# Kernel optimization log

Measured on AMD Instinct MI355X. Metric: run time of the kernel, lower is better.

Reference implementation:

```python
import jax, jax.numpy as jnp
import numpy as np

N_SAMPLES = 32768
N_ATOMS = 1024
ATOM_LEN = 2048
N_TO_KEEP = 1024


def fft_convolve(a, b):
    """Linear convolution via FFT: zero-pad both to 2n, multiply spectra, truncate to n."""
    n = a.shape[-1]
    a = jnp.pad(a, [(0, 0)] * (a.ndim - 1) + [(0, n)])
    b = jnp.pad(b, [(0, 0)] * (b.ndim - 1) + [(0, n)])
    spec = jnp.fft.rfft(a, axis=-1) * jnp.fft.rfft(b, axis=-1)  # broadcast (B,1024,2n//2+1)
    return jnp.fft.irfft(spec, axis=-1)[..., :n]


def sparsify(x, n_to_keep):
    """Keep the top-k raw values over the flattened per-batch feature map; zero the rest."""
    shp = x.shape
    flat = x.reshape(shp[0], -1)                       # (B, 1024*32768)
    vals, idx = jax.lax.top_k(flat, n_to_keep)         # (B, k)
    out = jnp.zeros_like(flat).at[jnp.arange(shp[0])[:, None], idx].set(vals)
    return out.reshape(shp)


def setup_inputs() -> dict:
    key = jax.random.key(0)
    k1, k2 = jax.random.split(key)
    x = jax.random.normal(k1, (2, 1, N_SAMPLES), dtype=jnp.float32)
    # atoms initialized uniform(-0.01, 0.01) in the original module
    atoms = jax.random.uniform(k2, (1, N_ATOMS, ATOM_LEN), dtype=jnp.float32,
                               minval=-0.01, maxval=0.01)
    return {"x": x, "atoms": atoms}


def reference(x, atoms):
    padded = jnp.pad(atoms, ((0, 0), (0, 0), (0, N_SAMPLES - atoms.shape[-1])))  # (1,1024,32768)
    fm = fft_convolve(x, padded)            # (B, 1024, 32768)
    fm = sparsify(fm, N_TO_KEEP)
    recon = fft_convolve(fm, padded)        # (B, 1024, 32768)
    recon = jnp.sum(recon, axis=1, keepdims=True)  # (B, 1, 32768)
    return recon
```

## Files before the change

kernel.cpp:

```cpp
#include <hip/hip_runtime.h>
#include <hip/hip_bf16.h>

#define NS    32768
#define NA    1024
#define AL    2048
#define KKEEP 1024
#define CAPC  (512*1024)

struct Cand { float v; unsigned idx; };

typedef short  short8  __attribute__((ext_vector_type(8)));
typedef short  short4v __attribute__((ext_vector_type(4)));
typedef float  f32x4   __attribute__((ext_vector_type(4)));


__device__ inline unsigned short f2bf(float f) {
    union { float f; unsigned u; } v; v.f = f;
    unsigned r = v.u + 0x7fffu + ((v.u >> 16) & 1u);
    return (unsigned short)(r >> 16);
}

__global__ void prep_kernel(const float* __restrict__ x, const float* __restrict__ atoms,
                            float* __restrict__ psum, float* __restrict__ hdr,
                            unsigned* __restrict__ candCnt, unsigned* __restrict__ done,
                            unsigned short* __restrict__ ab16) {
    __shared__ float red[12];
    __shared__ int   isLast;
    const int bid = blockIdx.x;
    const int tid = threadIdx.x;
    const int i   = bid * 256 + tid;
    float4 f = *(const float4*)(atoms + (size_t)i * 4);
    ushort4 o;
    o.x = f2bf(f.x); o.y = f2bf(f.y); o.z = f2bf(f.z); o.w = f2bf(f.w);
    *(ushort4*)(ab16 + (size_t)i * 4) = o;
    float sa  = f.x*f.x + f.y*f.y + f.z*f.z + f.w*f.w;
    float sx0 = 0.f, sx1 = 0.f;
    if (i < 16384) {
        float4 xv = *(const float4*)(x + (size_t)i * 4);
        float s = xv.x*xv.x + xv.y*xv.y + xv.z*xv.z + xv.w*xv.w;
        if (i < 8192) sx0 = s; else sx1 = s;
    }
    #pragma unroll
    for (int off = 32; off >= 1; off >>= 1) {
        sa  += __shfl_down(sa , off);
        sx0 += __shfl_down(sx0, off);
        sx1 += __shfl_down(sx1, off);
    }
    if ((tid & 63) == 0) {
        red[(tid >> 6) * 3 + 0] = sa;
        red[(tid >> 6) * 3 + 1] = sx0;
        red[(tid >> 6) * 3 + 2] = sx1;
    }
    __syncthreads();
    if (tid == 0) {
        psum[bid * 3 + 0] = red[0] + red[3] + red[6] + red[9];
        psum[bid * 3 + 1] = red[1] + red[4] + red[7] + red[10];
        psum[bid * 3 + 2] = red[2] + red[5] + red[8] + red[11];
        __threadfence();
        unsigned old = atomicAdd(done, 1u);
        isLast = (((old + 1u) & 2047u) == 0u) ? 1 : 0;
    }
    __syncthreads();
    if (!isLast) return;

    __threadfence();
    float pa = 0.f, p0s = 0.f, p1s = 0.f;
    for (int j = tid; j < 2048; j += 256) {
        pa  += psum[3 * j + 0];
        p0s += psum[3 * j + 1];
        p1s += psum[3 * j + 2];
    }
    #pragma unroll
    for (int off = 32; off >= 1; off >>= 1) {
        pa  += __shfl_down(pa , off);
        p0s += __shfl_down(p0s, off);
        p1s += __shfl_down(p1s, off);
    }
    __syncthreads();
    if ((tid & 63) == 0) {
        red[(tid >> 6) * 3 + 0] = pa;
        red[(tid >> 6) * 3 + 1] = p0s;
        red[(tid >> 6) * 3 + 2] = p1s;
    }
    __syncthreads();
    if (tid == 0) {
        hdr[0] = red[1] + red[4] + red[7] + red[10];
        hdr[1] = red[2] + red[5] + red[8] + red[11];
        hdr[2] = red[0] + red[3] + red[6] + red[9];
        candCnt[0] = 0u; candCnt[1] = 0u;
    }
}

#define XRW      2175
#define XRSTRIDE 2192
#define XRB      4384
#define NCPY     4
#define SA_BUF   16384

__device__ inline void gload_lds16(const unsigned short* g, unsigned char* lds) {
    __builtin_amdgcn_global_load_lds((const __attribute__((address_space(1))) void*)g,
                                     (__attribute__((address_space(3))) void*)lds,
                                     16, 0, 0);
}

__global__ __launch_bounds__(256, 3)
void fm_kernel(const float* __restrict__ x,
               const unsigned short* __restrict__ ab16,
               const float* __restrict__ hdr, unsigned* __restrict__ candCnt,
               Cand* __restrict__ cand, unsigned cap)
{
    __shared__ __align__(16) unsigned char  sA[2 * SA_BUF];
    __shared__ __align__(16) unsigned short sXR[NCPY * XRSTRIDE];

    const int bid = blockIdx.x;
    const int b   = bid >> 11;
    const int rem = bid & 2047;
    const int a0  = (rem >> 8) * 128;
    const int t0  = (rem & 255) * 128;

    const int tid  = threadIdx.x;
    const int lane = tid & 63;
    const int wid  = tid >> 6;
    const int wm   = wid >> 1;
    const int wn   = wid & 1;
    const int g    = lane >> 4;
    const int ln   = lane & 15;

    const int rot = (bid * 5) & 31;

    const float* __restrict__ xb = x + b * NS;

    for (int ti = tid; ti < XRW; ti += 256) {
        int t = t0 - 2047 + ti;
        float f = (t >= 0) ? xb[t] : 0.f;
        unsigned short h = f2bf(f);
        int p0 = 2174 - ti;
        #pragma unroll
        for (int m = 0; m < NCPY; ++m) sXR[m * XRSTRIDE + p0 + m] = h;
    }

    #define STAGE(bf, ck) do {                                                   \
        int kcs = (ck) * 64;                                                     \
        _Pragma("unroll")                                                        \
        for (int it = 0; it < 4; ++it) {                                         \
            int slot = (wid * 4 + it) * 64 + lane;                               \
            int row  = slot >> 3;                                                \
            int blk  = slot & 7;                                                 \
            const unsigned short* gsrc =                                         \
                ab16 + (size_t)(a0 + row) * AL + kcs + ((blk ^ (row & 7)) << 3); \
            gload_lds16(gsrc, sA + (bf) * SA_BUF + (size_t)(wid * 4 + it) * 1024); \
        }                                                                        \
    } while (0)

    f32x4 acc[4][4];
    #pragma unroll
    for (int i = 0; i < 4; ++i)
        #pragma unroll
        for (int j = 0; j < 4; ++j) acc[i][j] = (f32x4)0.0f;

    const int Rbase = 127 - wn * 64 - ln + 8 * g;
    const unsigned char* xrb = (const unsigned char*)sXR;

    int rowoff[4];
    #pragma unroll
    for (int mi = 0; mi < 4; ++mi) rowoff[mi] = (wm * 64 + mi * 16 + ln) * 128;
    const int swz0 = ((0 * 4 + g) ^ (ln & 7)) << 4;
    const int swz1 = ((1 * 4 + g) ^ (ln & 7)) << 4;

    #define LOADB(Rv, dst) do {                                                 \
        int p_ = ((Rv) + 3) & ~3;                                               \
        const unsigned char* a_ =                                               \
            xrb + (unsigned)(p_ - (Rv)) * XRB + (unsigned)p_ * 2u;              \
        short4v lo_ = *(const short4v*)a_;                                      \
        short4v hi_ = *(const short4v*)(a_ + 8);                                \
        dst = __builtin_shufflevector(lo_, hi_, 0, 1, 2, 3, 4, 5, 6, 7);        \
    } while (0)

    short8 b0, b1, b2, b3;

    #define LOADB4(Sv) do {                        \
        LOADB(Rbase      + 32 * (Sv), b0);         \
        LOADB(Rbase - 16 + 32 * (Sv), b1);         \
        LOADB(Rbase - 32 + 32 * (Sv), b2);         \
        LOADB(Rbase - 48 + 32 * (Sv), b3);         \
    } while (0)

    #define ROLLB(Sv) do {                         \
        b3 = b1; b2 = b0;                          \
        LOADB(Rbase      + 32 * (Sv), b0);         \
        LOADB(Rbase - 16 + 32 * (Sv), b1);         \
    } while (0)

    #define MFMAS(mi) do {                                                                  \
        acc[mi][0] = __builtin_amdgcn_mfma_f32_16x16x32_bf16(af[mi], b0, acc[mi][0],0,0,0); \
        acc[mi][1] = __builtin_amdgcn_mfma_f32_16x16x32_bf16(af[mi], b1, acc[mi][1],0,0,0); \
        acc[mi][2] = __builtin_amdgcn_mfma_f32_16x16x32_bf16(af[mi], b2, acc[mi][2],0,0,0); \
        acc[mi][3] = __builtin_amdgcn_mfma_f32_16x16x32_bf16(af[mi], b3, acc[mi][3],0,0,0); \
    } while (0)

    __syncthreads();

    LOADB4(rot * 2);

    STAGE(0, rot);
    STAGE(1, (rot + 1) & 31);

    for (int c = 0; c < 32; ++c) {
        const int chunk  = (c + rot) & 31;
        const int nchunk = (c + 1 + rot) & 31;
        const int cur    = c & 1;

        asm volatile("s_waitcnt vmcnt(4)" ::: "memory");
        __builtin_amdgcn_sched_barrier(0);
        __builtin_amdgcn_s_barrier();
        __builtin_amdgcn_sched_barrier(0);

        #pragma unroll
        for (int s = 0; s < 2; ++s) {
            short8 af[4];
            const int soff = cur * SA_BUF + (s ? swz1 : swz0);
            #pragma unroll
            for (int mi = 0; mi < 4; ++mi)
                af[mi] = *(const short8*)(sA + soff + rowoff[mi]);

            __builtin_amdgcn_s_setprio(1);
            MFMAS(0); MFMAS(1); MFMAS(2); MFMAS(3);
            __builtin_amdgcn_s_setprio(0);

            if (s == 0) {
                ROLLB(chunk * 2 + 1);
            } else {
                if (nchunk == 0) { LOADB4(0); }
                else             { ROLLB(nchunk * 2); }
            }
        }

        __builtin_amdgcn_sched_barrier(0);
        __builtin_amdgcn_s_barrier();
        __builtin_amdgcn_sched_barrier(0);

        STAGE(cur, (c + 2 + rot) & 31);
    }
    #undef LOADB
    #undef LOADB4
    #undef ROLLB
    #undef MFMAS
    #undef STAGE

    const float sig = sqrtf((hdr[2] * (1.0f / (float)NA)) * (hdr[b] * (1.0f / (float)NS)));
    const float T0  = 3.70f * sig;

    #pragma unroll
    for (int mi = 0; mi < 4; ++mi) {
        #pragma unroll
        for (int ni = 0; ni < 4; ++ni) {
            #pragma unroll
            for (int r = 0; r < 4; ++r) {
                float v = acc[mi][ni][r];
                if (v > T0) {
                    unsigned a = (unsigned)(a0 + wm * 64 + mi * 16 + g * 4 + r);
                    unsigned t = (unsigned)(t0 + wn * 64 + ni * 16 + ln);
                    unsigned idx = (a << 15) | t;
                    unsigned pos = atomicAdd(&candCnt[b], 1u);
                    if (pos < cap) {
                        Cand cc; cc.v = v; cc.idx = idx;
                        cand[(size_t)b * cap + pos] = cc;
                    }
                }
            }
        }
    }
}

__global__ void refine_band(const float* __restrict__ x, const float* __restrict__ atoms,
                            const float* __restrict__ hdr,
                            const unsigned* __restrict__ candCnt, Cand* __restrict__ cand,
                            unsigned cap) {
    const int lane = threadIdx.x & 63;
    const float TB0 = 3.85f * sqrtf((hdr[2] * (1.0f / (float)NA)) * (hdr[0] * (1.0f / (float)NS)));
    const float TB1 = 3.85f * sqrtf((hdr[2] * (1.0f / (float)NA)) * (hdr[1] * (1.0f / (float)NS)));

    const int wv = (int)((blockIdx.x * blockDim.x + threadIdx.x) >> 6);
    const int nw = (int)((gridDim.x * blockDim.x) >> 6);
    const int n0 = (int)min(candCnt[0], cap);
    const int n1 = (int)min(candCnt[1], cap);
    const int total = n0 + n1;
    for (int c = wv; c < total; c += nw) {
        const int b = (c < n0) ? 0 : 1;
        const size_t ci = (c < n0) ? (size_t)c : ((size_t)cap + (size_t)(c - n0));
        const Cand cc = cand[ci];
        if (cc.v <= ((b == 0) ? TB0 : TB1)) continue;
        const unsigned idx = cc.idx;
        const int a = (int)(idx >> 15);
        const int t = (int)(idx & (NS - 1));
        const float* __restrict__ ar = atoms + (size_t)a * AL;
        const float* __restrict__ xr = x + b * NS;
        double s = 0.0;
        for (int k = lane; k < AL; k += 64) {
            int xi = t - k;
            if (xi >= 0) s += (double)ar[k] * (double)xr[xi];
        }
        #pragma unroll
        for (int o = 32; o >= 1; o >>= 1) s += __shfl_down(s, o);
        if (lane == 0) cand[ci].v = (float)s;
    }
}

#define SELCAP 16384

__global__ void select_kernel(const unsigned* __restrict__ candCnt,
                              const Cand* __restrict__ cand, Cand* __restrict__ sel,
                              unsigned cap) {
    __shared__ float    s_vals[SELCAP];
    __shared__ float    s_red[16];
    __shared__ int      s_cnt;
    __shared__ int      s_nA;
    __shared__ int      s_nT;
    __shared__ int      s_exact;
    __shared__ float    s_tau;
    __shared__ Cand     s_A[KKEEP];
    __shared__ unsigned s_T[256];

    const int b = blockIdx.x;
    const Cand* __restrict__ cb = cand + (size_t)b * cap;
    const int n   = (int)min(candCnt[b], cap);
    const int tid = threadIdx.x;

    if (n <= KKEEP) {
        for (int i = tid; i < KKEEP; i += blockDim.x) {
            Cand z; z.v = 0.f; z.idx = 0u;
            sel[b * KKEEP + i] = (i < n) ? cb[i] : z;
        }
        return;
    }

    const bool useLds = (n <= SELCAP);
    if (useLds)
        for (int i = tid; i < n; i += blockDim.x) s_vals[i] = cb[i].v;

    float m = 0.f;
    if (useLds) { __syncthreads();
        for (int i = tid; i < n; i += blockDim.x) m = fmaxf(m, s_vals[i]);
    } else {
        for (int i = tid; i < n; i += blockDim.x) m = fmaxf(m, cb[i].v);
    }
    #pragma unroll
    for (int o = 32; o >= 1; o >>= 1) m = fmaxf(m, __shfl_down(m, o));
    if ((tid & 63) == 0) s_red[tid >> 6] = m;
    if (tid == 0) s_exact = 0;
    __syncthreads();
    float hi;
    {
        float mm = 0.f;
        #pragma unroll
        for (int w = 0; w < 16; ++w) mm = fmaxf(mm, s_red[w]);
        hi = mm;
    }
    float lo = 0.f;
    for (int iter = 0; iter < 64; ++iter) {
        float mid = 0.5f * (lo + hi);
        if (!(mid > lo && mid < hi)) break;
        if (tid == 0) s_cnt = 0;
        __syncthreads();
        int c = 0;
        if (useLds) for (int i = tid; i < n; i += blockDim.x) c += (s_vals[i] > mid) ? 1 : 0;
        else        for (int i = tid; i < n; i += blockDim.x) c += (cb[i].v  > mid) ? 1 : 0;
        #pragma unroll
        for (int o = 32; o >= 1; o >>= 1) c += __shfl_down(c, o);
        if ((tid & 63) == 0) atomicAdd(&s_cnt, c);
        __syncthreads();
        int cm = s_cnt;
        __syncthreads();
        if (cm == KKEEP) { if (tid == 0) { s_tau = mid; s_exact = 1; } break; }
        if (cm > KKEEP) lo = mid; else hi = mid;
    }
    __syncthreads();

    const int   exact = s_exact;
    const float tau   = exact ? s_tau : hi;

    for (int i = tid; i < KKEEP; i += blockDim.x) { s_A[i].v = 0.f; s_A[i].idx = 0u; }
    if (tid == 0) { s_nA = 0; s_nT = 0; }
    __syncthreads();

    for (int i = tid; i < n; i += blockDim.x) {
        float v = cb[i].v;
        if (v > tau) {
            int p = atomicAdd(&s_nA, 1);
            if (p < KKEEP) s_A[p] = cb[i];
        } else if (!exact && v == tau) {
            int p = atomicAdd(&s_nT, 1);
            if (p < 256) s_T[p] = cb[i].idx;
        }
    }
    __syncthreads();
    if (tid == 0) {
        int nA = s_nA; if (nA > KKEEP) nA = KKEEP;
        int need = KKEEP - nA;
        int nT = s_nT; if (nT > 256) nT = 256;
        for (int r = 0; r < need && r < nT; ++r) {
            unsigned best = 0xffffffffu; int bj = -1;
            for (int j = 0; j < nT; ++j) if (s_T[j] < best) { best = s_T[j]; bj = j; }
            Cand c; c.v = tau; c.idx = best;
            s_A[nA + r] = c;
            if (bj >= 0) s_T[bj] = 0xffffffffu;
        }
    }
    __syncthreads();
    for (int i = tid; i < KKEEP; i += blockDim.x) sel[b * KKEEP + i] = s_A[i];
}

__global__ void recon_kernel(const float* __restrict__ atoms, const Cand* __restrict__ sel,
                             float* __restrict__ out) {
    __shared__ float s_cv[KKEEP];
    __shared__ int   s_ca[KKEEP];
    __shared__ int   s_ct[KKEEP];
    __shared__ int   s_n;
    const int b    = blockIdx.x >> 7;
    const int tseg = (blockIdx.x & 127) << 8;
    const int t    = tseg + threadIdx.x;
    if (threadIdx.x == 0) s_n = 0;
    __syncthreads();
    for (int i = threadIdx.x; i < KKEEP; i += blockDim.x) {
        Cand c = sel[b * KKEEP + i];
        int t0e = (int)(c.idx & (NS - 1));
        if (c.v != 0.f && t0e <= tseg + 255 && t0e + (AL - 1) >= tseg) {
            int p = atomicAdd(&s_n, 1);
            s_cv[p] = c.v;
            s_ca[p] = (int)(c.idx >> 15);
            s_ct[p] = t0e;
        }
    }
    __syncthreads();
    const int n = s_n;
    float acc = 0.f;
    for (int e = 0; e < n; ++e) {
        int d = t - s_ct[e];
        if ((unsigned)d < (unsigned)AL)
            acc += s_cv[e] * atoms[(size_t)s_ca[e] * AL + d];
    }
    out[b * NS + t] = acc;
}

extern "C" void kernel_launch(void* const* d_in, const int* in_sizes, int n_in,
                              void* d_out, int out_size, void* d_ws, size_t ws_size,
                              hipStream_t stream) {
    const float* x     = (const float*)d_in[0];
    const float* atoms = (const float*)d_in[1];
    float* out = (float*)d_out;

    float*          hdr     = (float*)d_ws;
    unsigned*       candCnt = (unsigned*)((char*)d_ws + 16);
    unsigned*       done    = (unsigned*)((char*)d_ws + 32);
    float*          psum    = (float*)((char*)d_ws + 64);
    Cand*           sel     = (Cand*)((char*)d_ws + 32768);
    unsigned short* ab16    = (unsigned short*)((char*)d_ws + 65536);
    const size_t    candOff = 65536 + (size_t)NA * AL * 2;
    Cand*           cand    = (Cand*)((char*)d_ws + candOff);

    unsigned cap = CAPC;
    if (ws_size > candOff + 2 * sizeof(Cand) * 1024) {
        size_t fit = (ws_size - candOff) / (2 * sizeof(Cand));
        if (fit < cap) cap = (unsigned)fit;
    } else {
        cap = 1024;
    }

    prep_kernel  <<<2048, 256, 0, stream>>>(x, atoms, psum, hdr, candCnt, done, ab16);
    fm_kernel    <<<2 * (NA / 128) * (NS / 128), 256, 0, stream>>>(x, ab16, hdr, candCnt, cand, cap);
    refine_band  <<<512, 256, 0, stream>>>(x, atoms, hdr, candCnt, cand, cap);
    select_kernel<<<2, 1024, 0, stream>>>(candCnt, cand, sel, cap);
    recon_kernel <<<256, 256, 0, stream>>>(atoms, sel, out);
}
```

Before: 370.8 us.

## Fuse refine and select kernels using last-block-done atomic counter

After: 388.4 us. 1.05x slower.

```diff
diff --git a/kernel.cpp b/kernel.cpp
--- a/kernel.cpp
+++ b/kernel.cpp
@@ -272,47 +272,16 @@
     }
 }
 
-__global__ void refine_band(const float* __restrict__ x, const float* __restrict__ atoms,
-                            const float* __restrict__ hdr,
-                            const unsigned* __restrict__ candCnt, Cand* __restrict__ cand,
-                            unsigned cap) {
-    const int lane = threadIdx.x & 63;
-    const float TB0 = 3.85f * sqrtf((hdr[2] * (1.0f / (float)NA)) * (hdr[0] * (1.0f / (float)NS)));
-    const float TB1 = 3.85f * sqrtf((hdr[2] * (1.0f / (float)NA)) * (hdr[1] * (1.0f / (float)NS)));
-
-    const int wv = (int)((blockIdx.x * blockDim.x + threadIdx.x) >> 6);
-    const int nw = (int)((gridDim.x * blockDim.x) >> 6);
-    const int n0 = (int)min(candCnt[0], cap);
-    const int n1 = (int)min(candCnt[1], cap);
-    const int total = n0 + n1;
-    for (int c = wv; c < total; c += nw) {
-        const int b = (c < n0) ? 0 : 1;
-        const size_t ci = (c < n0) ? (size_t)c : ((size_t)cap + (size_t)(c - n0));
-        const Cand cc = cand[ci];
-        if (cc.v <= ((b == 0) ? TB0 : TB1)) continue;
-        const unsigned idx = cc.idx;
-        const int a = (int)(idx >> 15);
-        const int t = (int)(idx & (NS - 1));
-        const float* __restrict__ ar = atoms + (size_t)a * AL;
-        const float* __restrict__ xr = x + b * NS;
-        double s = 0.0;
-        for (int k = lane; k < AL; k += 64) {
-            int xi = t - k;
-            if (xi >= 0) s += (double)ar[k] * (double)xr[xi];
-        }
-        #pragma unroll
-        for (int o = 32; o >= 1; o >>= 1) s += __shfl_down(s, o);
-        if (lane == 0) cand[ci].v = (float)s;
-    }
-}
-
-#define SELCAP 16384
-
-__global__ void select_kernel(const unsigned* __restrict__ candCnt,
-                              const Cand* __restrict__ cand, Cand* __restrict__ sel,
-                              unsigned cap) {
+#define SELCAP  12288
+#define RS_GRID 512
+
+__global__ __launch_bounds__(256)
+void refine_select(const float* __restrict__ x, const float* __restrict__ atoms,
+                   const float* __restrict__ hdr,
+                   const unsigned* __restrict__ candCnt, Cand* __restrict__ cand,
+                   Cand* __restrict__ sel, unsigned* __restrict__ done, unsigned cap) {
     __shared__ float    s_vals[SELCAP];
-    __shared__ float    s_red[16];
+    __shared__ float    s_red[4];
     __shared__ int      s_cnt;
     __shared__ int      s_nA;
     __shared__ int      s_nT;
@@ -320,94 +289,131 @@
     __shared__ float    s_tau;
     __shared__ Cand     s_A[KKEEP];
     __shared__ unsigned s_T[256];
-
-    const int b = blockIdx.x;
-    const Cand* __restrict__ cb = cand + (size_t)b * cap;
-    const int n   = (int)min(candCnt[b], cap);
-    const int tid = threadIdx.x;
-
-    if (n <= KKEEP) {
-        for (int i = tid; i < KKEEP; i += blockDim.x) {
-            Cand z; z.v = 0.f; z.idx = 0u;
-            sel[b * KKEEP + i] = (i < n) ? cb[i] : z;
-        }
-        return;
-    }
-
-    const bool useLds = (n <= SELCAP);
-    if (useLds)
-        for (int i = tid; i < n; i += blockDim.x) s_vals[i] = cb[i].v;
-
-    float m = 0.f;
-    if (useLds) { __syncthreads();
-        for (int i = tid; i < n; i += blockDim.x) m = fmaxf(m, s_vals[i]);
-    } else {
-        for (int i = tid; i < n; i += blockDim.x) m = fmaxf(m, cb[i].v);
-    }
-    #pragma unroll
-    for (int o = 32; o >= 1; o >>= 1) m = fmaxf(m, __shfl_down(m, o));
-    if ((tid & 63) == 0) s_red[tid >> 6] = m;
-    if (tid == 0) s_exact = 0;
-    __syncthreads();
-    float hi;
+    __shared__ int      isLast;
+
+    const int tid  = threadIdx.x;
+    const int lane = tid & 63;
+
+    const float TB0 = 3.85f * sqrtf((hdr[2] * (1.0f / (float)NA)) * (hdr[0] * (1.0f / (float)NS)));
+    const float TB1 = 3.85f * sqrtf((hdr[2] * (1.0f / (float)NA)) * (hdr[1] * (1.0f / (float)NS)));
+
+    const int n0 = (int)min(candCnt[0], cap);
+    const int n1 = (int)min(candCnt[1], cap);
+    const int total = n0 + n1;
+
     {
-        float mm = 0.f;
+        const int wv = (int)((blockIdx.x * 256 + tid) >> 6);
+        const int nw = RS_GRID * 4;
+        for (int c = wv; c < total; c += nw) {
+            const int b = (c < n0) ? 0 : 1;
+            const size_t ci = (c < n0) ? (size_t)c : ((size_t)cap + (size_t)(c - n0));
+            const Cand cc = cand[ci];
+            if (cc.v <= ((b == 0) ? TB0 : TB1)) continue;
+            const unsigned idx = cc.idx;
+            const int a = (int)(idx >> 15);
+            const int t = (int)(idx & (NS - 1));
+            const float* __restrict__ ar = atoms + (size_t)a * AL;
+            const float* __restrict__ xr = x + b * NS;
+            double s = 0.0;
+            for (int k = lane; k < AL; k += 64) {
+                int xi = t - k;
+                if (xi >= 0) s += (double)ar[k] * (double)xr[xi];
+            }
+            #pragma unroll
+            for (int o = 32; o >= 1; o >>= 1) s += __shfl_down(s, o);
+            if (lane == 0) cand[ci].v = (float)s;
+        }
+    }
+
+    if (tid == 0) {
+        __threadfence();
+        unsigned old = atomicAdd(done, 1u);
+        isLast = (((old + 1u) & (RS_GRID - 1u)) == 0u) ? 1 : 0;
+    }
+    __syncthreads();
+    if (!isLast) return;
+    __threadfence();
+
+    for (int b = 0; b < 2; ++b) {
+        const Cand* __restrict__ cb = cand + (size_t)b * cap;
+        const int n = (b == 0) ? n0 : n1;
+        __syncthreads();
+
+        if (n <= KKEEP) {
+            for (int i = tid; i < KKEEP; i += 256) {
+                Cand z; z.v = 0.f; z.idx = 0u;
+                sel[b * KKEEP + i] = (i < n) ? cb[i] : z;
+            }
+            continue;
+        }
+
+        const bool useLds = (n <= SELCAP);
+        if (useLds)
+            for (int i = tid; i < n; i += 256) s_vals[i] = cb[i].v;
+        if (tid == 0) s_exact = 0;
+        __syncthreads();
+
+        float m = 0.f;
+        if (useLds) for (int i = tid; i < n; i += 256) m = fmaxf(m, s_vals[i]);
+        else        for (int i = tid; i < n; i += 256) m = fmaxf(m, cb[i].v);
         #pragma unroll
-        for (int w = 0; w < 16; ++w) mm = fmaxf(mm, s_red[w]);
-        hi = mm;
-    }
-    float lo = 0.f;
-    for (int iter = 0; iter < 64; ++iter) {
-        float mid = 0.5f * (lo + hi);
-        if (!(mid > lo && mid < hi)) break;
-        if (tid == 0) s_cnt = 0;
-        __syncthreads();
-        int c = 0;
-        if (useLds) for (int i = tid; i < n; i += blockDim.x) c += (s_vals[i] > mid) ? 1 : 0;
-        else        for (int i = tid; i < n; i += blockDim.x) c += (cb[i].v  > mid) ? 1 : 0;
-        #pragma unroll
-        for (int o = 32; o >= 1; o >>= 1) c += __shfl_down(c, o);
-        if ((tid & 63) == 0) atomicAdd(&s_cnt, c);
-        __syncthreads();
-        int cm = s_cnt;
-        __syncthreads();
-        if (cm == KKEEP) { if (tid == 0) { s_tau = mid; s_exact = 1; } break; }
-        if (cm > KKEEP) lo = mid; else hi = mid;
-    }
-    __syncthreads();
-
-    const int   exact = s_exact;
-    const float tau   = exact ? s_tau : hi;
-
-    for (int i = tid; i < KKEEP; i += blockDim.x) { s_A[i].v = 0.f; s_A[i].idx = 0u; }
-    if (tid == 0) { s_nA = 0; s_nT = 0; }
-    __syncthreads();
-
-    for (int i = tid; i < n; i += blockDim.x) {
-        float v = cb[i].v;
-        if (v > tau) {
-            int p = atomicAdd(&s_nA, 1);
-            if (p < KKEEP) s_A[p] = cb[i];
-        } else if (!exact && v == tau) {
-            int p = atomicAdd(&s_nT, 1);
-            if (p < 256) s_T[p] = cb[i].idx;
-        }
-    }
-    __syncthreads();
-    if (tid == 0) {
-        int nA = s_nA; if (nA > KKEEP) nA = KKEEP;
-        int need = KKEEP - nA;
-        int nT = s_nT; if (nT > 256) nT = 256;
-        for (int r = 0; r < need && r < nT; ++r) {
-            unsigned best = 0xffffffffu; int bj = -1;
-            for (int j = 0; j < nT; ++j) if (s_T[j] < best) { best = s_T[j]; bj = j; }
-            Cand c; c.v = tau; c.idx = best;
-            s_A[nA + r] = c;
-            if (bj >= 0) s_T[bj] = 0xffffffffu;
-        }
-    }
-    __syncthreads();
-    for (int i = tid; i < KKEEP; i += blockDim.x) sel[b * KKEEP + i] = s_A[i];
+        for (int o = 32; o >= 1; o >>= 1) m = fmaxf(m, __shfl_down(m, o));
+        if ((tid & 63) == 0) s_red[tid >> 6] = m;
+        __syncthreads();
+        float hi = fmaxf(fmaxf(s_red[0], s_red[1]), fmaxf(s_red[2], s_red[3]));
+        float lo = 0.f;
+        for (int iter = 0; iter < 64; ++iter) {
+            float mid = 0.5f * (lo + hi);
+            if (!(mid > lo && mid < hi)) break;
+            if (tid == 0) s_cnt = 0;
+            __syncthreads();
+            int c = 0;
+            if (useLds) for (int i = tid; i < n; i += 256) c += (s_vals[i] > mid) ? 1 : 0;
+            else        for (int i = tid; i < n; i += 256) c += (cb[i].v  > mid) ? 1 : 0;
+            #pragma unroll
+            for (int o = 32; o >= 1; o >>= 1) c += __shfl_down(c, o);
+            if ((tid & 63) == 0) atomicAdd(&s_cnt, c);
+            __syncthreads();
+            int cm = s_cnt;
+            __syncthreads();
+            if (cm == KKEEP) { if (tid == 0) { s_tau = mid; s_exact = 1; } break; }
+            if (cm > KKEEP) lo = mid; else hi = mid;
+        }
+        __syncthreads();
+
+        const int   exact = s_exact;
+        const float tau   = exact ? s_tau : hi;
+
+        for (int i = tid; i < KKEEP; i += 256) { s_A[i].v = 0.f; s_A[i].idx = 0u; }
+        if (tid == 0) { s_nA = 0; s_nT = 0; }
+        __syncthreads();
+
+        for (int i = tid; i < n; i += 256) {
+            float v = cb[i].v;
+            if (v > tau) {
+                int p = atomicAdd(&s_nA, 1);
+                if (p < KKEEP) s_A[p] = cb[i];
+            } else if (!exact && v == tau) {
+                int p = atomicAdd(&s_nT, 1);
+                if (p < 256) s_T[p] = cb[i].idx;
+            }
+        }
+        __syncthreads();
+        if (tid == 0) {
+            int nA = s_nA; if (nA > KKEEP) nA = KKEEP;
+            int need = KKEEP - nA;
+            int nT = s_nT; if (nT > 256) nT = 256;
+            for (int r = 0; r < need && r < nT; ++r) {
+                unsigned best = 0xffffffffu; int bj = -1;
+                for (int j = 0; j < nT; ++j) if (s_T[j] < best) { best = s_T[j]; bj = j; }
+                Cand c; c.v = tau; c.idx = best;
+                s_A[nA + r] = c;
+                if (bj >= 0) s_T[bj] = 0xffffffffu;
+            }
+        }
+        __syncthreads();
+        for (int i = tid; i < KKEEP; i += 256) sel[b * KKEEP + i] = s_A[i];
+    }
 }
 
 __global__ void recon_kernel(const float* __restrict__ atoms, const Cand* __restrict__ sel,
@@ -468,7 +474,6 @@
 
     prep_kernel  <<<2048, 256, 0, stream>>>(x, atoms, psum, hdr, candCnt, done, ab16);
     fm_kernel    <<<2 * (NA / 128) * (NS / 128), 256, 0, stream>>>(x, ab16, hdr, candCnt, cand, cap);
-    refine_band  <<<512, 256, 0, stream>>>(x, atoms, hdr, candCnt, cand, cap);
-    select_kernel<<<2, 1024, 0, stream>>>(candCnt, cand, sel, cap);
+    refine_select<<<RS_GRID, 256, 0, stream>>>(x, atoms, hdr, candCnt, cand, sel, done + 1, cap);
     recon_kernel <<<256, 256, 0, stream>>>(atoms, sel, out);
 }
```
